# Performance work log

Hardware: AMD Instinct MI355X
Metric: run time of the kernel (lower is better)

The kernel has to match this reference:

```python
import jax, jax.numpy as jnp
import numpy as np

B, S, T = 512, 1024, 48  # batch, seq_len, num_tags


def setup_inputs() -> dict:
    key = jax.random.key(0)
    k1, k2, k3, k4, k5, k6 = jax.random.split(key, 6)
    emissions = jax.random.normal(k1, (B, S, T), dtype=jnp.float32)
    tags = jax.random.randint(k2, (B, S), 0, T)
    lengths = jax.random.randint(k3, (B,), 1, S + 1)
    mask = jnp.arange(S)[None, :] < lengths[:, None]  # contiguous prefix mask, bool
    # learned parameters (nn.Parameter zeros init in the module; use small random here)
    start_transitions = 0.01 * jax.random.normal(k4, (T,), dtype=jnp.float32)
    end_transitions = 0.01 * jax.random.normal(k5, (T,), dtype=jnp.float32)
    transitions = 0.01 * jax.random.normal(k6, (T, T), dtype=jnp.float32)
    return {
        "emissions": emissions,
        "tags": tags,
        "mask": mask,
        "start_transitions": start_transitions,
        "end_transitions": end_transitions,
        "transitions": transitions,
    }


def _log_partition(emissions, mask, start_transitions, end_transitions, transitions):
    # score[b, i] = log-sum over paths ending in tag i (note: this repo indexes
    # transitions[i, j] with j = previous tag inside the partition recursion).
    score0 = start_transitions[None, :] + emissions[:, 0]  # (B, T)

    def step(score, xs):
        emit_t, mask_t = xs  # (B, T), (B,)
        # score_t[b, i] = logsumexp_j(score[b, j] + transitions[i, j]) + emit_t[b, i]
        score_t = jax.nn.logsumexp(score[:, None, :] + transitions[None, :, :], axis=2) + emit_t
        score = jnp.where(mask_t[:, None], score_t, score)
        return score, None

    em = jnp.swapaxes(emissions[:, 1:], 0, 1)  # (S-1, B, T)
    mk = jnp.swapaxes(mask[:, 1:], 0, 1)       # (S-1, B)
    score, _ = jax.lax.scan(step, score0, (em, mk))
    return jax.nn.logsumexp(score + end_transitions[None, :], axis=1)  # (B,)


def _score_sentence(emissions, tags, mask, start_transitions, end_transitions, transitions):
    Bb = emissions.shape[0]
    bidx = jnp.arange(Bb)
    maskf = mask.astype(emissions.dtype)
    score = start_transitions[tags[:, 0]] + emissions[bidx, 0, tags[:, 0]]  # (B,)
    trans_sc = transitions[tags[:, :-1], tags[:, 1:]]  # (B, S-1)
    emit_sc = jnp.take_along_axis(emissions, tags[:, :, None], axis=2)[..., 0]  # (B, S)
    score = score + jnp.sum((trans_sc + emit_sc[:, 1:]) * maskf[:, 1:], axis=1)
    last_idx = jnp.sum(mask.astype(jnp.int32), axis=1) - 1  # (B,)
    last_tags = jnp.take_along_axis(tags, last_idx[:, None], axis=1)[:, 0]
    return score + end_transitions[last_tags]


def reference(emissions, tags, mask, start_transitions, end_transitions, transitions):
    log_denominator = _log_partition(emissions, mask, start_transitions, end_transitions, transitions)
    log_numerator = _score_sentence(emissions, tags, mask, start_transitions, end_transitions, transitions)
    return jnp.mean(log_denominator - log_numerator)
```

## Files before the change

### kernel.cpp

```cpp
#include <hip/hip_runtime.h>

#define BB 512
#define SS 1024
#define TT 48
#define GG 16
#define CK 8
#define NSLOT 5

typedef __attribute__((ext_vector_type(8))) short short8;
typedef __attribute__((ext_vector_type(4))) float float4v;

__device__ __forceinline__ unsigned short f2bf(float x) {
    unsigned u = __float_as_uint(x);
    u += 0x7FFFu + ((u >> 16) & 1u);
    return (unsigned short)(u >> 16);
}
__device__ __forceinline__ unsigned pk2bf(float lo, float hi) {
#if __has_builtin(__builtin_amdgcn_cvt_pk_bf16_f32)
    typedef __bf16 bf16x2 __attribute__((ext_vector_type(2)));
    union { bf16x2 v; unsigned u; } cv;
    cv.v = __builtin_amdgcn_cvt_pk_bf16_f32(lo, hi);
    return cv.u;
#else
    return __builtin_amdgcn_perm(__float_as_uint(hi) + 0x8000u,
                                 __float_as_uint(lo) + 0x8000u, 0x07060302u);
#endif
}
__device__ __forceinline__ float bflo(unsigned u) { return __uint_as_float(u << 16); }
__device__ __forceinline__ float bfhi(unsigned u) { return __uint_as_float(u & 0xFFFF0000u); }
__device__ __forceinline__ float wave_sum(float v) {
#pragma unroll
    for (int off = 32; off >= 1; off >>= 1) v += __shfl_xor(v, off, 64);
    return v;
}
__device__ __forceinline__ int wave_sum_i(int v) {
#pragma unroll
    for (int off = 32; off >= 1; off >>= 1) v += __shfl_xor(v, off, 64);
    return v;
}

__global__ __launch_bounds__(256)
void crf_numer(const float* __restrict__ em, const int* __restrict__ tags,
               const int* __restrict__ mask, const float* __restrict__ start_tr,
               const float* __restrict__ end_tr, const float* __restrict__ trans,
               float* __restrict__ numer, int* __restrict__ lenArr) {
    const int b = blockIdx.x, tid = threadIdx.x;
    const float* emb = em + (size_t)b * SS * TT;
    const int* tg = tags + (size_t)b * SS;
    const int* mk = mask + (size_t)b * SS;
    int cnt = 0; float ns = 0.f;
    for (int s = tid; s < SS; s += 256) {
        int m = mk[s];
        cnt += (m != 0);
        if (s >= 1 && m) {
            int tp = tg[s - 1], tc = tg[s];
            ns += trans[tp * TT + tc] + emb[s * TT + tc];
        }
    }
    float wsum = wave_sum(ns);
    int wcnt = wave_sum_i(cnt);
    __shared__ float sf[4]; __shared__ int si[4];
    if ((tid & 63) == 0) { sf[tid >> 6] = wsum; si[tid >> 6] = wcnt; }
    __syncthreads();
    if (tid == 0) {
        float tot = sf[0] + sf[1] + sf[2] + sf[3];
        int L = si[0] + si[1] + si[2] + si[3];
        int t0 = tg[0];
        tot += start_tr[t0] + emb[t0] + end_tr[tg[L - 1]];
        numer[b] = tot;
        lenArr[b] = L;
    }
}

__global__ __launch_bounds__(320, 1)
void crf_fwd(const float* __restrict__ em, const float* __restrict__ start_tr,
             const float* __restrict__ end_tr, const float* __restrict__ trans,
             const int* __restrict__ lenArr, float* __restrict__ denomArr) {
    __shared__ uint2 ring[NSLOT * CK * 3 * 64];

    const int tid = threadIdx.x;
    const int wave = tid >> 6, lane = tid & 63;
    const int wgbase = blockIdx.x * GG;

    if (wave == 0) {
        const int n = lane & 15, q = lane >> 4;
        const int bb = wgbase + n;

        short8 afr[3][2];
#pragma unroll
        for (int mt = 0; mt < 3; ++mt) {
            const int so = mt * 16 + n;
#pragma unroll
            for (int kt = 0; kt < 2; ++kt) {
                short8 a;
#pragma unroll
                for (int i = 0; i < 8; ++i) {
                    int si_;
                    if (kt == 0) si_ = (i < 4) ? (q * 4 + i) : (16 + q * 4 + (i - 4));
                    else         si_ = (i < 4) ? (32 + q * 4 + i) : -1;
                    a[i] = (si_ >= 0) ? (short)f2bf(__expf(trans[so * TT + si_])) : (short)0;
                }
                afr[mt][kt] = a;
            }
        }

        const float* em0 = em + (size_t)bb * SS * TT + q * 4;
        float p[3][4];
#pragma unroll
        for (int mt = 0; mt < 3; ++mt) {
            float4 v = *(const float4*)(em0 + mt * 16);
            int sb = mt * 16 + q * 4;
            p[mt][0] = __expf(start_tr[sb + 0] + v.x);
            p[mt][1] = __expf(start_tr[sb + 1] + v.y);
            p[mt][2] = __expf(start_tr[sb + 2] + v.z);
            p[mt][3] = __expf(start_tr[sb + 3] + v.w);
        }

        const int len = lenArr[bb];
        int Lmax = len;
#pragma unroll
        for (int off = 1; off < 64; off <<= 1) {
            int o = __shfl_xor(Lmax, off, 64);
            Lmax = Lmax > o ? Lmax : o;
        }
        const int P = (Lmax + 6) >> 3;

        bool cc0 = (len == 1);
        float dc[3][4];
#pragma unroll
        for (int mt = 0; mt < 3; ++mt)
#pragma unroll
            for (int r = 0; r < 4; ++r) dc[mt][r] = cc0 ? p[mt][r] : 0.f;
        float lcap = 0.f, logscale = 0.f;
        const float4v Z = {0.f, 0.f, 0.f, 0.f};

        for (int pp = -3; pp < P; ++pp) {
            if (pp >= 0) {
                const uint2* rp = &ring[(pp % NSLOT) * (CK * 3 * 64) + lane];
                uint2 c0 = rp[0], c1 = rp[64], c2v = rp[128];
#pragma unroll
                for (int u = 0; u < 8; ++u) {
                    uint2 n0, n1, n2;
                    if (u < 7) {
                        n0 = rp[(u + 1) * 192];
                        n1 = rp[(u + 1) * 192 + 64];
                        n2 = rp[(u + 1) * 192 + 128];
                    }
                    union { short8 v; unsigned w[4]; } B0, B1;
                    B0.w[0] = pk2bf(p[0][0], p[0][1]); B0.w[1] = pk2bf(p[0][2], p[0][3]);
                    B0.w[2] = pk2bf(p[1][0], p[1][1]); B0.w[3] = pk2bf(p[1][2], p[1][3]);
                    B1.w[0] = pk2bf(p[2][0], p[2][1]); B1.w[1] = pk2bf(p[2][2], p[2][3]);
                    B1.w[2] = 0u; B1.w[3] = 0u;
                    float4v A0 = __builtin_amdgcn_mfma_f32_16x16x32_bf16(afr[0][0], B0.v, Z, 0, 0, 0);
                    float4v A1 = __builtin_amdgcn_mfma_f32_16x16x32_bf16(afr[1][0], B0.v, Z, 0, 0, 0);
                    float4v A2 = __builtin_amdgcn_mfma_f32_16x16x32_bf16(afr[2][0], B0.v, Z, 0, 0, 0);
                    A0 = __builtin_amdgcn_mfma_f32_16x16x32_bf16(afr[0][1], B1.v, A0, 0, 0, 0);
                    A1 = __builtin_amdgcn_mfma_f32_16x16x32_bf16(afr[1][1], B1.v, A1, 0, 0, 0);
                    A2 = __builtin_amdgcn_mfma_f32_16x16x32_bf16(afr[2][1], B1.v, A2, 0, 0, 0);
                    p[0][0] = A0[0] * bflo(c0.x); p[0][1] = A0[1] * bfhi(c0.x);
                    p[0][2] = A0[2] * bflo(c0.y); p[0][3] = A0[3] * bfhi(c0.y);
                    p[1][0] = A1[0] * bflo(c1.x); p[1][1] = A1[1] * bfhi(c1.x);
                    p[1][2] = A1[2] * bflo(c1.y); p[1][3] = A1[3] * bfhi(c1.y);
                    p[2][0] = A2[0] * bflo(c2v.x); p[2][1] = A2[1] * bfhi(c2v.x);
                    p[2][2] = A2[2] * bflo(c2v.y); p[2][3] = A2[3] * bfhi(c2v.y);
                    bool cc = (len == 8 * pp + u + 2);
#pragma unroll
                    for (int mt = 0; mt < 3; ++mt)
#pragma unroll
                        for (int r = 0; r < 4; ++r) dc[mt][r] = cc ? p[mt][r] : dc[mt][r];
                    lcap = cc ? logscale : lcap;
                    c0 = n0; c1 = n1; c2v = n2;
                    if (u == 7) {
                        float m = fmaxf(p[0][0], p[0][1]);
                        m = fmaxf(m, fmaxf(p[0][2], p[0][3]));
                        m = fmaxf(m, fmaxf(p[1][0], p[1][1]));
                        m = fmaxf(m, fmaxf(p[1][2], p[1][3]));
                        m = fmaxf(m, fmaxf(p[2][0], p[2][1]));
                        m = fmaxf(m, fmaxf(p[2][2], p[2][3]));
                        m = fmaxf(m, __shfl_xor(m, 16, 64));
                        m = fmaxf(m, __shfl_xor(m, 32, 64));
                        m = fmaxf(m, 1e-30f);
                        logscale += __logf(m);
                        float rm = __builtin_amdgcn_rcpf(m);
#pragma unroll
                        for (int mt = 0; mt < 3; ++mt)
#pragma unroll
                            for (int r = 0; r < 4; ++r) p[mt][r] *= rm;
                    }
                }
            }
            __builtin_amdgcn_s_barrier();
        }

        float pe = 0.f;
#pragma unroll
        for (int mt = 0; mt < 3; ++mt) {
            int sb = mt * 16 + q * 4;
            pe = fmaf(dc[mt][0], __expf(end_tr[sb + 0]), pe);
            pe = fmaf(dc[mt][1], __expf(end_tr[sb + 1]), pe);
            pe = fmaf(dc[mt][2], __expf(end_tr[sb + 2]), pe);
            pe = fmaf(dc[mt][3], __expf(end_tr[sb + 3]), pe);
        }
        pe += __shfl_xor(pe, 16, 64);
        pe += __shfl_xor(pe, 32, 64);
        if (lane < 16) denomArr[bb] = lcap + __logf(pe);

    } else {
        const int T = (wave - 1) >> 1;
        const int sub = (wave - 1) & 1;
        const int nb = lane & 15, q4 = lane >> 4;
        const int bb = wgbase + nb;
        const int len_v = lenArr[bb];
        int Lmax = len_v;
#pragma unroll
        for (int off = 1; off < 64; off <<= 1) {
            int o = __shfl_xor(Lmax, off, 64);
            Lmax = Lmax > o ? Lmax : o;
        }
        const int P = (Lmax + 6) >> 3;

        const float* emP = em + (size_t)bb * SS * TT + q4 * 4;
        float4 buf[12];

        for (int pp = -3; pp < P; ++pp) {
            int cv = pp + 1;
            if (cv >= 0 && cv < P && (cv & 1) == T) {
                uint2* wp = &ring[(cv % NSLOT) * (CK * 3 * 64) + lane];
#pragma unroll
                for (int k = 0; k < 12; ++k) {
                    const int i = sub * 12 + k, u = i / 3, j = i % 3;
                    int t = 1 + 8 * cv + u;
                    bool live = t < len_v;
                    float4 v = buf[k];
                    unsigned ox = pk2bf(__expf(v.x), __expf(v.y));
                    unsigned oy = pk2bf(__expf(v.z), __expf(v.w));
                    uint2 o;
                    o.x = live ? ox : 0u;
                    o.y = live ? oy : 0u;
                    wp[u * 192 + j * 64] = o;
                }
            }
            int ci = pp + 3;
            if (ci < P && (ci & 1) == T) {
#pragma unroll
                for (int k = 0; k < 12; ++k) {
                    const int i = sub * 12 + k, u = i / 3, j = i % 3;
                    int t = 1 + 8 * ci + u; t = t < SS ? t : SS - 1;
                    buf[k] = *(const float4*)(emP + (size_t)t * TT + j * 16);
                }
            }
            __builtin_amdgcn_s_waitcnt(0xC07F);
            __builtin_amdgcn_s_barrier();
        }
    }
}

__global__ __launch_bounds__(64)
void crf_reduce(const float* __restrict__ denom, const float* __restrict__ numer,
                float* __restrict__ out) {
    int lane = threadIdx.x;
    float s = 0.f;
    for (int i = lane; i < BB; i += 64) s += denom[i] - numer[i];
    s = wave_sum(s);
    if (lane == 0) out[0] = s * (1.0f / (float)BB);
}

extern "C" void kernel_launch(void* const* d_in, const int* in_sizes, int n_in,
                              void* d_out, int out_size, void* d_ws, size_t ws_size,
                              hipStream_t stream) {
    const float* emissions = (const float*)d_in[0];
    const int*   tags      = (const int*)d_in[1];
    const int*   mask      = (const int*)d_in[2];
    const float* start_tr  = (const float*)d_in[3];
    const float* end_tr    = (const float*)d_in[4];
    const float* trans     = (const float*)d_in[5];

    char* ws = (char*)d_ws;
    float* denom = (float*)ws;
    float* numer = (float*)(ws + 2048);
    int*   lenA  = (int*)(ws + 4096);

    crf_numer<<<BB, 256, 0, stream>>>(emissions, tags, mask, start_tr, end_tr,
                                      trans, numer, lenA);
    crf_fwd<<<BB / GG, 320, 0, stream>>>(emissions, start_tr, end_tr, trans,
                                         lenA, denom);
    crf_reduce<<<1, 64, 0, stream>>>(denom, numer, (float*)d_out);
}
```

Baseline: 321.6 us.

## Shorten forward-recursion critical path with independent MFMAs and permlane swaps

The serial forward recursion now issues all six MFMAs independently (two partial sums added afterwards) instead of chaining accumulators, which shortens the dependent latency per step. The end-state capture moves before the p update, with a final check after the loop, and the ring reads for the next step are issued after the MFMAs. Cross-group max and sum reductions use permlane16/32 swap builtins instead of shuffles, and the scan wave gets raised scheduling priority. The numerator kernel is also vectorised to int4 loads, with one chunk of four positions per thread. The reordered capture logic is a correctness risk if the indexing shift is wrong.

```diff
diff --git a/kernel.cpp b/kernel.cpp
--- a/kernel.cpp
+++ b/kernel.cpp
@@ -9,6 +9,7 @@
 
 typedef __attribute__((ext_vector_type(8))) short short8;
 typedef __attribute__((ext_vector_type(4))) float float4v;
+typedef unsigned uint2v __attribute__((ext_vector_type(2)));
 
 __device__ __forceinline__ unsigned short f2bf(float x) {
     unsigned u = __float_as_uint(x);
@@ -38,6 +39,30 @@
     for (int off = 32; off >= 1; off >>= 1) v += __shfl_xor(v, off, 64);
     return v;
 }
+__device__ __forceinline__ float xgrp_max(float m) {
+#if __has_builtin(__builtin_amdgcn_permlane16_swap) && __has_builtin(__builtin_amdgcn_permlane32_swap)
+    uint2v a = __builtin_amdgcn_permlane16_swap(__float_as_uint(m), __float_as_uint(m), false, false);
+    m = fmaxf(__uint_as_float(a[0]), __uint_as_float(a[1]));
+    uint2v b = __builtin_amdgcn_permlane32_swap(__float_as_uint(m), __float_as_uint(m), false, false);
+    m = fmaxf(__uint_as_float(b[0]), __uint_as_float(b[1]));
+#else
+    m = fmaxf(m, __shfl_xor(m, 16, 64));
+    m = fmaxf(m, __shfl_xor(m, 32, 64));
+#endif
+    return m;
+}
+__device__ __forceinline__ float xgrp_sum(float m) {
+#if __has_builtin(__builtin_amdgcn_permlane16_swap) && __has_builtin(__builtin_amdgcn_permlane32_swap)
+    uint2v a = __builtin_amdgcn_permlane16_swap(__float_as_uint(m), __float_as_uint(m), false, false);
+    m = __uint_as_float(a[0]) + __uint_as_float(a[1]);
+    uint2v b = __builtin_amdgcn_permlane32_swap(__float_as_uint(m), __float_as_uint(m), false, false);
+    m = __uint_as_float(b[0]) + __uint_as_float(b[1]);
+#else
+    m += __shfl_xor(m, 16, 64);
+    m += __shfl_xor(m, 32, 64);
+#endif
+    return m;
+}
 
 __global__ __launch_bounds__(256)
 void crf_numer(const float* __restrict__ em, const int* __restrict__ tags,
@@ -48,15 +73,16 @@
     const float* emb = em + (size_t)b * SS * TT;
     const int* tg = tags + (size_t)b * SS;
     const int* mk = mask + (size_t)b * SS;
-    int cnt = 0; float ns = 0.f;
-    for (int s = tid; s < SS; s += 256) {
-        int m = mk[s];
-        cnt += (m != 0);
-        if (s >= 1 && m) {
-            int tp = tg[s - 1], tc = tg[s];
-            ns += trans[tp * TT + tc] + emb[s * TT + tc];
-        }
-    }
+    const int s0 = tid * 4;
+    const int4 t4 = *(const int4*)(tg + s0);
+    const int4 m4 = *(const int4*)(mk + s0);
+    const int tprev = (tid == 0) ? 0 : tg[s0 - 1];
+    int cnt = (m4.x != 0) + (m4.y != 0) + (m4.z != 0) + (m4.w != 0);
+    float ns = 0.f;
+    if (tid > 0 && m4.x) ns += trans[tprev * TT + t4.x] + emb[(size_t)s0 * TT + t4.x];
+    if (m4.y) ns += trans[t4.x * TT + t4.y] + emb[(size_t)(s0 + 1) * TT + t4.y];
+    if (m4.z) ns += trans[t4.y * TT + t4.z] + emb[(size_t)(s0 + 2) * TT + t4.z];
+    if (m4.w) ns += trans[t4.z * TT + t4.w] + emb[(size_t)(s0 + 3) * TT + t4.w];
     float wsum = wave_sum(ns);
     int wcnt = wave_sum_i(cnt);
     __shared__ float sf[4]; __shared__ int si[4];
@@ -83,6 +109,7 @@
     const int wgbase = blockIdx.x * GG;
 
     if (wave == 0) {
+        __builtin_amdgcn_s_setprio(1);
         const int n = lane & 15, q = lane >> 4;
         const int bb = wgbase + n;
 
@@ -125,12 +152,11 @@
         }
         const int P = (Lmax + 6) >> 3;
 
-        bool cc0 = (len == 1);
         float dc[3][4];
 #pragma unroll
         for (int mt = 0; mt < 3; ++mt)
 #pragma unroll
-            for (int r = 0; r < 4; ++r) dc[mt][r] = cc0 ? p[mt][r] : 0.f;
+            for (int r = 0; r < 4; ++r) dc[mt][r] = 0.f;
         float lcap = 0.f, logscale = 0.f;
         const float4v Z = {0.f, 0.f, 0.f, 0.f};
 
@@ -140,45 +166,44 @@
                 uint2 c0 = rp[0], c1 = rp[64], c2v = rp[128];
 #pragma unroll
                 for (int u = 0; u < 8; ++u) {
+                    union { short8 v; unsigned w[4]; } B0, B1;
+                    B0.w[0] = pk2bf(p[0][0], p[0][1]); B0.w[1] = pk2bf(p[0][2], p[0][3]);
+                    B0.w[2] = pk2bf(p[1][0], p[1][1]); B0.w[3] = pk2bf(p[1][2], p[1][3]);
+                    B1.w[0] = pk2bf(p[2][0], p[2][1]); B1.w[1] = pk2bf(p[2][2], p[2][3]);
+                    B1.w[2] = 0u; B1.w[3] = 0u;
+                    float4v A0a = __builtin_amdgcn_mfma_f32_16x16x32_bf16(afr[0][0], B0.v, Z, 0, 0, 0);
+                    float4v A1a = __builtin_amdgcn_mfma_f32_16x16x32_bf16(afr[1][0], B0.v, Z, 0, 0, 0);
+                    float4v A2a = __builtin_amdgcn_mfma_f32_16x16x32_bf16(afr[2][0], B0.v, Z, 0, 0, 0);
+                    float4v A0b = __builtin_amdgcn_mfma_f32_16x16x32_bf16(afr[0][1], B1.v, Z, 0, 0, 0);
+                    float4v A1b = __builtin_amdgcn_mfma_f32_16x16x32_bf16(afr[1][1], B1.v, Z, 0, 0, 0);
+                    float4v A2b = __builtin_amdgcn_mfma_f32_16x16x32_bf16(afr[2][1], B1.v, Z, 0, 0, 0);
                     uint2 n0, n1, n2;
                     if (u < 7) {
                         n0 = rp[(u + 1) * 192];
                         n1 = rp[(u + 1) * 192 + 64];
                         n2 = rp[(u + 1) * 192 + 128];
                     }
-                    union { short8 v; unsigned w[4]; } B0, B1;
-                    B0.w[0] = pk2bf(p[0][0], p[0][1]); B0.w[1] = pk2bf(p[0][2], p[0][3]);
-                    B0.w[2] = pk2bf(p[1][0], p[1][1]); B0.w[3] = pk2bf(p[1][2], p[1][3]);
-                    B1.w[0] = pk2bf(p[2][0], p[2][1]); B1.w[1] = pk2bf(p[2][2], p[2][3]);
-                    B1.w[2] = 0u; B1.w[3] = 0u;
-                    float4v A0 = __builtin_amdgcn_mfma_f32_16x16x32_bf16(afr[0][0], B0.v, Z, 0, 0, 0);
-                    float4v A1 = __builtin_amdgcn_mfma_f32_16x16x32_bf16(afr[1][0], B0.v, Z, 0, 0, 0);
-                    float4v A2 = __builtin_amdgcn_mfma_f32_16x16x32_bf16(afr[2][0], B0.v, Z, 0, 0, 0);
-                    A0 = __builtin_amdgcn_mfma_f32_16x16x32_bf16(afr[0][1], B1.v, A0, 0, 0, 0);
-                    A1 = __builtin_amdgcn_mfma_f32_16x16x32_bf16(afr[1][1], B1.v, A1, 0, 0, 0);
-                    A2 = __builtin_amdgcn_mfma_f32_16x16x32_bf16(afr[2][1], B1.v, A2, 0, 0, 0);
-                    p[0][0] = A0[0] * bflo(c0.x); p[0][1] = A0[1] * bfhi(c0.x);
-                    p[0][2] = A0[2] * bflo(c0.y); p[0][3] = A0[3] * bfhi(c0.y);
-                    p[1][0] = A1[0] * bflo(c1.x); p[1][1] = A1[1] * bfhi(c1.x);
-                    p[1][2] = A1[2] * bflo(c1.y); p[1][3] = A1[3] * bfhi(c1.y);
-                    p[2][0] = A2[0] * bflo(c2v.x); p[2][1] = A2[1] * bfhi(c2v.x);
-                    p[2][2] = A2[2] * bflo(c2v.y); p[2][3] = A2[3] * bfhi(c2v.y);
-                    bool cc = (len == 8 * pp + u + 2);
+                    float e00 = bflo(c0.x),  e01 = bfhi(c0.x),  e02 = bflo(c0.y),  e03 = bfhi(c0.y);
+                    float e10 = bflo(c1.x),  e11 = bfhi(c1.x),  e12 = bflo(c1.y),  e13 = bfhi(c1.y);
+                    float e20 = bflo(c2v.x), e21 = bfhi(c2v.x), e22 = bflo(c2v.y), e23 = bfhi(c2v.y);
+                    bool cc = (len == 8 * pp + u + 1);
 #pragma unroll
                     for (int mt = 0; mt < 3; ++mt)
 #pragma unroll
                         for (int r = 0; r < 4; ++r) dc[mt][r] = cc ? p[mt][r] : dc[mt][r];
                     lcap = cc ? logscale : lcap;
+                    p[0][0] = (A0a[0] + A0b[0]) * e00; p[0][1] = (A0a[1] + A0b[1]) * e01;
+                    p[0][2] = (A0a[2] + A0b[2]) * e02; p[0][3] = (A0a[3] + A0b[3]) * e03;
+                    p[1][0] = (A1a[0] + A1b[0]) * e10; p[1][1] = (A1a[1] + A1b[1]) * e11;
+                    p[1][2] = (A1a[2] + A1b[2]) * e12; p[1][3] = (A1a[3] + A1b[3]) * e13;
+                    p[2][0] = (A2a[0] + A2b[0]) * e20; p[2][1] = (A2a[1] + A2b[1]) * e21;
+                    p[2][2] = (A2a[2] + A2b[2]) * e22; p[2][3] = (A2a[3] + A2b[3]) * e23;
                     c0 = n0; c1 = n1; c2v = n2;
                     if (u == 7) {
-                        float m = fmaxf(p[0][0], p[0][1]);
-                        m = fmaxf(m, fmaxf(p[0][2], p[0][3]));
-                        m = fmaxf(m, fmaxf(p[1][0], p[1][1]));
-                        m = fmaxf(m, fmaxf(p[1][2], p[1][3]));
-                        m = fmaxf(m, fmaxf(p[2][0], p[2][1]));
-                        m = fmaxf(m, fmaxf(p[2][2], p[2][3]));
-                        m = fmaxf(m, __shfl_xor(m, 16, 64));
-                        m = fmaxf(m, __shfl_xor(m, 32, 64));
+                        float m = fmaxf(fmaxf(p[0][0], p[0][1]), fmaxf(p[0][2], p[0][3]));
+                        m = fmaxf(m, fmaxf(fmaxf(p[1][0], p[1][1]), fmaxf(p[1][2], p[1][3])));
+                        m = fmaxf(m, fmaxf(fmaxf(p[2][0], p[2][1]), fmaxf(p[2][2], p[2][3])));
+                        m = xgrp_max(m);
                         m = fmaxf(m, 1e-30f);
                         logscale += __logf(m);
                         float rm = __builtin_amdgcn_rcpf(m);
@@ -190,6 +215,14 @@
                 }
             }
             __builtin_amdgcn_s_barrier();
+        }
+        {
+            bool cc = (len == 8 * P + 1);
+#pragma unroll
+            for (int mt = 0; mt < 3; ++mt)
+#pragma unroll
+                for (int r = 0; r < 4; ++r) dc[mt][r] = cc ? p[mt][r] : dc[mt][r];
+            lcap = cc ? logscale : lcap;
         }
 
         float pe = 0.f;
@@ -201,8 +234,7 @@
             pe = fmaf(dc[mt][2], __expf(end_tr[sb + 2]), pe);
             pe = fmaf(dc[mt][3], __expf(end_tr[sb + 3]), pe);
         }
-        pe += __shfl_xor(pe, 16, 64);
-        pe += __shfl_xor(pe, 32, 64);
+        pe = xgrp_sum(pe);
         if (lane < 16) denomArr[bb] = lcap + __logf(pe);
 
     } else {
```

Result: slower. 339.0 us (+5.4%).
